# Performance work log

Measured on AMD Instinct MI355X. Metric: run time of the kernel, lower is better.

## Reference

```python
import math
import jax, jax.numpy as jnp
import numpy as np

KV_SIZE = 960
EPS = 1e-5  # InstanceNorm2d default eps


def _instance_norm(x):
    # x: [B, H, C, K]; InstanceNorm2d(affine=False): normalize each (b,h) plane
    mu = x.mean(axis=(-2, -1), keepdims=True)
    var = x.var(axis=(-2, -1), keepdims=True)  # biased variance, matches torch
    return (x - mu) * jax.lax.rsqrt(var + EPS)


def _branch(emb, Wq, K, V, Wo):
    # emb: [B,N,C], Wq: [H,C,C], K/V: [B,H,N,KV], Wo: [C,C]
    Q = jnp.einsum('bnc,hdc->bhnd', emb, Wq)                       # per-head Linear
    scores = jnp.einsum('bhnc,bhnk->bhck', Q, K) / math.sqrt(KV_SIZE)
    probs = jax.nn.softmax(_instance_norm(scores), axis=-1)        # [B,H,C,KV]
    ctx = jnp.einsum('bhck,bhnk->bhcn', probs, V)                  # [B,H,C,N]
    ctx = ctx.mean(axis=1).transpose(0, 2, 1)                      # mean over heads -> [B,N,C]
    return ctx @ Wo.T                                              # out Linear (no bias)


def setup_inputs() -> dict:
    key = jax.random.key(0)
    ks = jax.random.split(key, 16)
    B, N, H = 8, 1024, 4
    C = [64, 128, 256, 512]
    d = {}
    for i, c in enumerate(C):
        d[f'emb{i+1}'] = jax.random.normal(ks[i], (B, N, c), dtype=jnp.float32)
    d['emb_all'] = jax.random.normal(ks[4], (B, N, KV_SIZE), dtype=jnp.float32)
    for i, c in enumerate(C):
        d[f'Wq{i+1}'] = jax.random.normal(ks[5 + i], (H, c, c), dtype=jnp.float32) * 0.02
    d['Wk'] = jax.random.normal(ks[9], (H, KV_SIZE, KV_SIZE), dtype=jnp.float32) * 0.02
    d['Wv'] = jax.random.normal(ks[10], (H, KV_SIZE, KV_SIZE), dtype=jnp.float32) * 0.02
    for i, c in enumerate(C):
        d[f'Wo{i+1}'] = jax.random.normal(ks[11 + i], (c, c), dtype=jnp.float32) * 0.02
    return d


def reference(emb1, emb2, emb3, emb4, emb_all,
              Wq1, Wq2, Wq3, Wq4, Wk, Wv,
              Wo1, Wo2, Wo3, Wo4):
    # shared K/V: per-head Linear over emb_all -> [B,H,N,KV]
    K = jnp.einsum('bnk,hjk->bhnj', emb_all, Wk)
    V = jnp.einsum('bnk,hjk->bhnj', emb_all, Wv)
    O1 = _branch(emb1, Wq1, K, V, Wo1)
    O2 = _branch(emb2, Wq2, K, V, Wo2)
    O3 = _branch(emb3, Wq3, K, V, Wo3)
    O4 = _branch(emb4, Wq4, K, V, Wo4)
    return (O1, O2, O3, O4)
```

## Files before the change

### kernel.cpp

```cpp
#include <hip/hip_runtime.h>
#include <stdint.h>

typedef unsigned short u16;
typedef short bf16x8 __attribute__((ext_vector_type(8)));
typedef float f32x4 __attribute__((ext_vector_type(4)));
typedef u16 u16x4 __attribute__((ext_vector_type(4)));

__device__ __forceinline__ u16 f2bf(float f) {
    unsigned u = __builtin_bit_cast(unsigned, f);
    unsigned r = (u + 0x7fffu + ((u >> 16) & 1u)) >> 16;
    return (u16)r;
}
__device__ __forceinline__ float bf2f(u16 h) {
    unsigned u = ((unsigned)h) << 16;
    return __builtin_bit_cast(float, u);
}

typedef const __attribute__((address_space(1))) unsigned int* gptr_t;
typedef __attribute__((address_space(3))) unsigned int* lptr_t;
__device__ __forceinline__ void gload16(const void* g, void* l) {
    __builtin_amdgcn_global_load_lds((gptr_t)(uintptr_t)g, (lptr_t)(uintptr_t)l, 16, 0, 0);
}

__device__ __constant__ int d_offs[4] = {0, 512, 768, 896};
__device__ __constant__ int d_cs[4] = {512, 256, 128, 64};

__global__ __launch_bounds__(256) void cast_bf16(const float4* __restrict__ in,
                                                 u16x4* __restrict__ out, int n4) {
    int i = blockIdx.x * 256 + threadIdx.x;
    if (i < n4) {
        float4 f = in[i];
        u16x4 o = {f2bf(f.x), f2bf(f.y), f2bf(f.z), f2bf(f.w)};
        out[i] = o;
    }
}

#define ARD(DST, BUFO, Q)                                                          \
    _Pragma("unroll") for (int f = 0; f < MFP; f++)                                \
        _Pragma("unroll") for (int kb = 0; kb < 2; kb++) {                         \
            int rl = ((Q)*MFP + f) * 16 + la;                                      \
            DST[f][kb] = *(const bf16x8*)&lds[(BUFO) + rl * 64 +                   \
                                              (((kb * 4 + lk4) ^ (rl & 7)) << 3)]; \
        }
#define BRD(BUFO)                                                                  \
    _Pragma("unroll") for (int ni = 0; ni < 4; ni++)                               \
        _Pragma("unroll") for (int kb = 0; kb < 2; kb++) {                         \
            int rl = brow0 + ni * 16 + la;                                         \
            breg[ni][kb] = *(const bf16x8*)&lds[(BUFO) + rl * 64 +                 \
                                                (((kb * 4 + lk4) ^ (rl & 7)) << 3)]; \
        }
#define MMA(Q, SRC)                                                                \
    __builtin_amdgcn_sched_barrier(0);                                             \
    __builtin_amdgcn_s_setprio(1);                                                 \
    _Pragma("unroll") for (int f = 0; f < MFP; f++)                                \
        _Pragma("unroll") for (int ni = 0; ni < 4; ni++)                           \
            _Pragma("unroll") for (int kb = 0; kb < 2; kb++)                       \
                acc[(Q)*MFP + f][ni] = __builtin_amdgcn_mfma_f32_16x16x32_bf16(    \
                    SRC[f][kb], breg[ni][kb], acc[(Q)*MFP + f][ni], 0, 0, 0);      \
    __builtin_amdgcn_s_setprio(0);
#define WAITL(N) asm volatile("s_waitcnt lgkmcnt(" #N ")" ::: "memory")
#define WLGA               \
    if constexpr (MFP == 2) \
        WAITL(4);           \
    else                    \
        WAITL(2);

template <int BM>
__global__ __launch_bounds__(512, 2) void gemm_nt_8ph(
    const u16* __restrict__ A, long sAb, long sAh, int lda,
    const u16* __restrict__ B, long sBb, long sBh, int ldb,
    u16* __restrict__ C, long sCb, long sCh, int ldc,
    int M, int N, int K, int hdiv, float alpha) {
    constexpr int NA = BM / 128;
    constexpr int MFP = BM / 128;
    constexpr int WTM = BM / 2;
    constexpr int NMF = WTM / 16;
    constexpr int APART = WTM * 64;
    constexpr int BPART = 128 * 64;
    constexpr int BUFSZ = 2 * APART + 2 * BPART;
    __shared__ u16 lds[2 * BUFSZ];

    int gx = gridDim.x, gy = gridDim.y;
    int nwg = gx * gy * gridDim.z;
    int orig = blockIdx.x + gx * (blockIdx.y + gy * blockIdx.z);
    int q = nwg >> 3, r = nwg & 7;
    int xcd = orig & 7, seq = orig >> 3;
    int wg = (xcd < r ? xcd * (q + 1) : r * (q + 1) + (xcd - r) * q) + seq;
    int bx = wg % gx, tmpw = wg / gx;
    int by = tmpw % gy, bz = tmpw / gy;

    int bb = bz / hdiv, hh = bz - bb * hdiv;
    const u16* Ab = A + (size_t)bb * sAb + (size_t)hh * sAh;
    const u16* Bb = B + (size_t)bb * sBb + (size_t)hh * sBh;
    u16* Cb = C + (size_t)bb * sCb + (size_t)hh * sCh;
    int tm = by * BM, tn = bx * 256;
    int t = threadIdx.x, lane = t & 63, w = t >> 6;
    int wm = w >> 2, wn = w & 3;
    int la = lane & 15, lk4 = lane >> 4;
    int brow0 = (wn & 1) * 64;

    const u16* pA0[NA];
    const u16* pA1[NA];
    const u16* pB0[2];
    const u16* pB1[2];
#pragma unroll
    for (int i = 0; i < NA; i++) {
        int seg = i * 512 + t;
        int col = (((seg & 7) ^ ((seg >> 3) & 7)) << 3);
        int r0 = tm + (seg >> 3);
        if (r0 > M - 1) r0 = M - 1;
        pA0[i] = Ab + (size_t)r0 * lda + col;
        int r1 = tm + WTM + (seg >> 3);
        if (r1 > M - 1) r1 = M - 1;
        pA1[i] = Ab + (size_t)r1 * lda + col;
    }
#pragma unroll
    for (int i = 0; i < 2; i++) {
        int seg = i * 512 + t;
        int col = (((seg & 7) ^ ((seg >> 3) & 7)) << 3);
        int r0 = tn + (seg >> 3);
        if (r0 > N - 1) r0 = N - 1;
        pB0[i] = Bb + (size_t)r0 * ldb + col;
        int r1 = tn + 128 + (seg >> 3);
        if (r1 > N - 1) r1 = N - 1;
        pB1[i] = Bb + (size_t)r1 * ldb + col;
    }

    auto AOF = [&](int buf, int h) { return buf * BUFSZ + h * APART; };
    auto BOF = [&](int buf, int h) { return buf * BUFSZ + 2 * APART + h * BPART; };
    auto stA0 = [&](int buf) {
#pragma unroll
        for (int i = 0; i < NA; i++) {
            gload16(pA0[i], &lds[AOF(buf, 0) + (i * 512 + t) * 8]);
            pA0[i] += 64;
        }
    };
    auto stA1 = [&](int buf) {
#pragma unroll
        for (int i = 0; i < NA; i++) {
            gload16(pA1[i], &lds[AOF(buf, 1) + (i * 512 + t) * 8]);
            pA1[i] += 64;
        }
    };
    auto stB0 = [&](int buf) {
#pragma unroll
        for (int i = 0; i < 2; i++) {
            gload16(pB0[i], &lds[BOF(buf, 0) + (i * 512 + t) * 8]);
            pB0[i] += 64;
        }
    };
    auto stB1 = [&](int buf) {
#pragma unroll
        for (int i = 0; i < 2; i++) {
            gload16(pB1[i], &lds[BOF(buf, 1) + (i * 512 + t) * 8]);
            pB1[i] += 64;
        }
    };

    int nt = K / 64;
    stA0(0);
    stA1(0);
    stB0(0);
    stB1(0);
    stB0(1);
    stB1(1);
    asm volatile("s_waitcnt vmcnt(4)" ::: "memory");
    __builtin_amdgcn_s_barrier();

    f32x4 acc[NMF][4] = {};
    bf16x8 breg[4][2];
    bf16x8 aregA[MFP][2], aregB[MFP][2];
    ARD(aregA, AOF(0, wm), 0)

    for (int k = 0; k < nt; ++k) {
        int buf = k & 1, nbuf = buf ^ 1;
        int ao = AOF(buf, wm), bo = BOF(buf, wn >> 1), aoN = AOF(nbuf, wm);
        bool s1 = (k + 1 < nt), s2 = (k + 2 < nt);
        {
            __builtin_amdgcn_s_barrier();
            BRD(bo)
            ARD(aregB, ao, 1)
            if (s1) stA0(nbuf);
            WLGA
            MMA(0, aregA)
        }
        {
            __builtin_amdgcn_s_barrier();
            ARD(aregA, ao, 2)
            if (s1) stA1(nbuf);
            WLGA
            MMA(1, aregB)
        }
        {
            __builtin_amdgcn_s_barrier();
            ARD(aregB, ao, 3)
            if (s2) stB0(buf);
            WLGA
            MMA(2, aregA)
            if (s2)
                asm volatile("s_waitcnt vmcnt(2)" ::: "memory");
            else
                asm volatile("s_waitcnt vmcnt(0)" ::: "memory");
        }
        {
            __builtin_amdgcn_s_barrier();
            if (s1) { ARD(aregA, aoN, 0) }
            if (s2) stB1(buf);
            if (s1) {
                WLGA
            } else {
                WAITL(0);
            }
            MMA(3, aregB)
        }
    }
#pragma unroll
    for (int mi = 0; mi < NMF; mi++)
#pragma unroll
        for (int ni = 0; ni < 4; ni++)
#pragma unroll
            for (int r_ = 0; r_ < 4; r_++) {
                int m = tm + wm * WTM + mi * 16 + ((lane >> 4) << 2) + r_;
                int n = tn + wn * 64 + ni * 16 + la;
                if (m < M && n < N)
                    Cb[(size_t)m * ldc + n] = f2bf(acc[mi][ni][r_] * alpha);
            }
}

template <typename OUT>
__global__ __launch_bounds__(256) void gemm_nt128(
    const u16* __restrict__ A, long sAb, long sAh, int lda,
    const u16* __restrict__ B, long sBb, long sBh, int ldb,
    OUT* __restrict__ C, long sCb, long sCh, int ldc,
    int M, int N, int K, int hdiv, float alpha) {
    __shared__ u16 sA[128 * 64];
    __shared__ u16 sB[128 * 64];
    int gx = gridDim.x, gy = gridDim.y;
    int nwg = gx * gy * gridDim.z;
    int orig = blockIdx.x + gx * (blockIdx.y + gy * blockIdx.z);
    int q = nwg >> 3, r = nwg & 7;
    int xcd = orig & 7, seq = orig >> 3;
    int wg = (xcd < r ? xcd * (q + 1) : r * (q + 1) + (xcd - r) * q) + seq;
    int bx = wg % gx, tmpw = wg / gx;
    int by = tmpw % gy, bz = tmpw / gy;

    int bb = bz / hdiv, hh = bz - bb * hdiv;
    const u16* Ab = A + (size_t)bb * sAb + (size_t)hh * sAh;
    const u16* Bb = B + (size_t)bb * sBb + (size_t)hh * sBh;
    OUT* Cb = C + (size_t)bb * sCb + (size_t)hh * sCh;
    int tm = by * 128, tn = bx * 128;
    int t = threadIdx.x, lane = t & 63, w = t >> 6;
    int wr = w >> 1, wc = w & 1;
    int r0 = t >> 3, c0 = (t & 7) * 8;
    const u16* gA[4];
    const u16* gB[4];
#pragma unroll
    for (int i = 0; i < 4; i++) {
        int ar = tm + i * 32 + r0;
        if (ar > M - 1) ar = M - 1;
        gA[i] = Ab + (size_t)ar * lda + c0;
    }
#pragma unroll
    for (int i = 0; i < 4; i++) {
        int br = tn + i * 32 + r0;
        if (br > N - 1) br = N - 1;
        gB[i] = Bb + (size_t)br * ldb + c0;
    }
    f32x4 acc[4][4] = {};
    int la = lane & 15, lk = (lane >> 4) * 8;
    for (int k0 = 0; k0 < K; k0 += 64) {
#pragma unroll
        for (int i = 0; i < 4; i++) {
            gload16(gA[i], &sA[(i * 256 + t) * 8]);
            gA[i] += 64;
        }
#pragma unroll
        for (int i = 0; i < 4; i++) {
            gload16(gB[i], &sB[(i * 256 + t) * 8]);
            gB[i] += 64;
        }
        __syncthreads();
#pragma unroll
        for (int kk = 0; kk < 64; kk += 32) {
            bf16x8 a[4], b[4];
#pragma unroll
            for (int mi = 0; mi < 4; mi++)
                a[mi] = *(const bf16x8*)&sA[(wr * 64 + mi * 16 + la) * 64 + kk + lk];
#pragma unroll
            for (int ni = 0; ni < 4; ni++)
                b[ni] = *(const bf16x8*)&sB[(wc * 64 + ni * 16 + la) * 64 + kk + lk];
#pragma unroll
            for (int mi = 0; mi < 4; mi++)
#pragma unroll
                for (int ni = 0; ni < 4; ni++)
                    acc[mi][ni] = __builtin_amdgcn_mfma_f32_16x16x32_bf16(
                        a[mi], b[ni], acc[mi][ni], 0, 0, 0);
        }
        __syncthreads();
    }
#pragma unroll
    for (int mi = 0; mi < 4; mi++)
#pragma unroll
        for (int ni = 0; ni < 4; ni++)
#pragma unroll
            for (int r_ = 0; r_ < 4; r_++) {
                int m = tm + wr * 64 + mi * 16 + (lane >> 4) * 4 + r_;
                int n = tn + wc * 64 + ni * 16 + la;
                if (m < M && n < N) {
                    float v = acc[mi][ni][r_] * alpha;
                    if constexpr (sizeof(OUT) == 4)
                        Cb[(size_t)m * ldc + n] = v;
                    else
                        Cb[(size_t)m * ldc + n] = f2bf(v);
                }
            }
}

__global__ __launch_bounds__(256) void in_stats1(const u16* __restrict__ sc,
                                                 double* __restrict__ part,
                                                 int G, int mode, int C) {
    int p = blockIdx.y, g = blockIdx.x, t = threadIdx.x;
    size_t base;
    int n8;
    if (mode) {
        int z = p >> 2, i = p & 3;
        base = (size_t)z * 921600 + (size_t)d_offs[i] * 960;
        n8 = d_cs[i] * 120;
    } else {
        base = (size_t)p * C * 960;
        n8 = C * 120;
    }
    const u16* x = sc + base;
    double s = 0.0, q = 0.0;
    for (int i = g * 256 + t; i < n8; i += G * 256) {
        u16x4 a = *(const u16x4*)&x[i * 8];
        u16x4 b = *(const u16x4*)&x[i * 8 + 4];
#pragma unroll
        for (int j = 0; j < 4; j++) {
            float fa = bf2f(a[j]), fb = bf2f(b[j]);
            s += (double)fa + (double)fb;
            q += (double)fa * fa + (double)fb * fb;
        }
    }
#pragma unroll
    for (int o = 32; o; o >>= 1) {
        s += __shfl_down(s, o);
        q += __shfl_down(q, o);
    }
    __shared__ double rs[4], rq[4];
    int w = t >> 6;
    if ((t & 63) == 0) {
        rs[w] = s;
        rq[w] = q;
    }
    __syncthreads();
    if (t == 0) {
        part[2 * ((size_t)p * G + g)] = rs[0] + rs[1] + rs[2] + rs[3];
        part[2 * ((size_t)p * G + g) + 1] = rq[0] + rq[1] + rq[2] + rq[3];
    }
}

__global__ __launch_bounds__(64) void in_stats2(const double* __restrict__ part,
                                                float* __restrict__ stats,
                                                int G, int mode, int C) {
    int p = blockIdx.x, t = threadIdx.x;
    int cnt = (mode ? d_cs[p & 3] : C) * 960;
    double s = 0.0, q = 0.0;
    if (t < G) {
        s = part[2 * ((size_t)p * G + t)];
        q = part[2 * ((size_t)p * G + t) + 1];
    }
#pragma unroll
    for (int o = 32; o; o >>= 1) {
        s += __shfl_down(s, o);
        q += __shfl_down(q, o);
    }
    if (t == 0) {
        float mu = (float)(s / cnt);
        float var = (float)(q / cnt) - mu * mu;
        stats[2 * p] = mu;
        stats[2 * p + 1] = rsqrtf(var + 1e-5f);
    }
}

__global__ __launch_bounds__(256) void norm_softmax_cat(const u16* __restrict__ sc,
                                                        const float* __restrict__ stats,
                                                        u16* __restrict__ prB) {
    int row = blockIdx.x;
    int z = row / 960, c = row - z * 960;
    int i = c < 512 ? 0 : (c < 768 ? 1 : (c < 896 ? 2 : 3));
    int plane = z * 4 + i;
    int b = z >> 2, h = z & 3;
    const u16* x = sc + (size_t)row * 960;
    u16* o = prB + (((size_t)b * 960 + c) * 4 + h) * 960;
    float mu = stats[2 * plane], rs = stats[2 * plane + 1];
    int t = threadIdx.x;
    bool act = t < 240;
    float v[4];
    float mx = -1e30f;
    if (act) {
        u16x4 d = *(const u16x4*)&x[t * 4];
#pragma unroll
        for (int j = 0; j < 4; j++) {
            v[j] = (bf2f(d[j]) - mu) * rs;
            mx = fmaxf(mx, v[j]);
        }
    }
    __shared__ float r1[4], r2[4];
#pragma unroll
    for (int o_ = 32; o_; o_ >>= 1) mx = fmaxf(mx, __shfl_xor(mx, o_));
    int w = t >> 6;
    if ((t & 63) == 0) r1[w] = mx;
    __syncthreads();
    mx = fmaxf(fmaxf(r1[0], r1[1]), fmaxf(r1[2], r1[3]));
    float s = 0.f;
    if (act) {
#pragma unroll
        for (int j = 0; j < 4; j++) {
            v[j] = __expf(v[j] - mx);
            s += v[j];
        }
    }
#pragma unroll
    for (int o_ = 32; o_; o_ >>= 1) s += __shfl_xor(s, o_);
    if ((t & 63) == 0) r2[w] = s;
    __syncthreads();
    s = r2[0] + r2[1] + r2[2] + r2[3];
    float inv = 1.0f / s;
    if (act) {
        u16x4 ov;
#pragma unroll
        for (int j = 0; j < 4; j++) ov[j] = f2bf(v[j] * inv);
        *(u16x4*)&o[t * 4] = ov;
    }
}

__global__ __launch_bounds__(256) void norm_softmax_ip(u16* sc,
                                                       const float* __restrict__ stats,
                                                       int C) {
    int row = blockIdx.x;
    int plane = row / C;
    u16* x = sc + (size_t)row * 960;
    float mu = stats[2 * plane], rs = stats[2 * plane + 1];
    int t = threadIdx.x;
    bool act = t < 240;
    float v[4];
    float mx = -1e30f;
    if (act) {
        u16x4 d = *(const u16x4*)&x[t * 4];
#pragma unroll
        for (int j = 0; j < 4; j++) {
            v[j] = (bf2f(d[j]) - mu) * rs;
            mx = fmaxf(mx, v[j]);
        }
    }
    __shared__ float r1[4], r2[4];
#pragma unroll
    for (int o = 32; o; o >>= 1) mx = fmaxf(mx, __shfl_xor(mx, o));
    int w = t >> 6;
    if ((t & 63) == 0) r1[w] = mx;
    __syncthreads();
    mx = fmaxf(fmaxf(r1[0], r1[1]), fmaxf(r1[2], r1[3]));
    float s = 0.f;
    if (act) {
#pragma unroll
        for (int j = 0; j < 4; j++) {
            v[j] = __expf(v[j] - mx);
            s += v[j];
        }
    }
#pragma unroll
    for (int o = 32; o; o >>= 1) s += __shfl_xor(s, o);
    if ((t & 63) == 0) r2[w] = s;
    __syncthreads();
    s = r2[0] + r2[1] + r2[2] + r2[3];
    float inv = 1.0f / s;
    if (act) {
        u16x4 o;
#pragma unroll
        for (int j = 0; j < 4; j++) o[j] = f2bf(v[j] * inv);
        *(u16x4*)&x[t * 4] = o;
    }
}

__global__ __launch_bounds__(256) void mean_heads(const u16* __restrict__ ctx, long ps,
                                                  u16* __restrict__ cm, int C) {
    int b = blockIdx.z;
    int n0 = blockIdx.x * 64, c0 = blockIdx.y * 64;
    __shared__ float sm[64][65];
    int t = threadIdx.x;
    float acc[16];
#pragma unroll
    for (int j = 0; j < 16; j++) acc[j] = 0.f;
    for (int h = 0; h < 4; h++) {
        const u16* p = ctx + (size_t)(b * 4 + h) * ps;
#pragma unroll
        for (int j = 0; j < 16; j++) {
            int lin = j * 256 + t;
            int cc = lin >> 6, nn = lin & 63;
            acc[j] += bf2f(p[(size_t)(c0 + cc) * 1024 + n0 + nn]);
        }
    }
#pragma unroll
    for (int j = 0; j < 16; j++) {
        int lin = j * 256 + t;
        sm[lin >> 6][lin & 63] = acc[j] * 0.25f;
    }
    __syncthreads();
#pragma unroll
    for (int j = 0; j < 16; j++) {
        int lin = j * 256 + t;
        int nn = lin >> 6, cc = lin & 63;
        cm[((size_t)b * 1024 + n0 + nn) * C + c0 + cc] = f2bf(sm[cc][nn]);
    }
}

extern "C" void kernel_launch(void* const* d_in, const int* in_sizes, int n_in,
                              void* d_out, int out_size, void* d_ws, size_t ws_size,
                              hipStream_t stream) {
    const int B = 8, NN = 1024, KV = 960;
    const int Cs[4] = {64, 128, 256, 512};
    const int ord[4] = {3, 2, 1, 0};
    const int offs[4] = {0, 512, 768, 896};
    const float* emb[4];
    for (int i = 0; i < 4; i++) emb[i] = (const float*)d_in[i];
    const float* embAll = (const float*)d_in[4];
    const float* Wq[4];
    for (int i = 0; i < 4; i++) Wq[i] = (const float*)d_in[5 + i];
    const float* Wk = (const float*)d_in[9];
    const float* Wv = (const float*)d_in[10];
    const float* Wo[4];
    for (int i = 0; i < 4; i++) Wo[i] = (const float*)d_in[11 + i];
    float* out = (float*)d_out;
    size_t outOff[4];
    {
        size_t o = 0;
        for (int i = 0; i < 4; i++) { outOff[i] = o; o += (size_t)B * NN * Cs[i]; }
    }

    const size_t SKV = 62914560;
    const size_t SSC = 58982400;
    const size_t SWQ = 2785280, SWO = 696320, SCM = 8388608;
    const size_t SPART = 131072, SST = 1024;
    const size_t SMALL = SWQ + SWO + SCM + SPART + SST;
    const size_t NEED_BAT = SSC + 3 * SKV + SMALL + 512;

    float invs = 1.0f / sqrtf((float)KV);
    auto g128 = [](int n) { return (n + 127) / 128; };

    if (ws_size >= NEED_BAT) {
        char* p = (char*)d_ws;
        u16* scB = (u16*)p;        p += SSC;
        u16* QtB = (u16*)p;        p += SKV;
        u16* Kt = (u16*)p;         p += SKV;
        u16* VbC = (u16*)p;        p += SKV;
        u16* wq[4];
        for (int i = 0; i < 4; i++) { wq[i] = (u16*)p; p += (size_t)4 * Cs[i] * Cs[i] * 2; }
        u16* wo[4];
        for (int i = 0; i < 4; i++) { wo[i] = (u16*)p; p += (size_t)Cs[i] * Cs[i] * 2; }
        u16* cmX = (u16*)p;        p += SCM;
        double* part = (double*)p; p += SPART;
        float* stats = (float*)p;

        u16* eA = scB;
        u16* wk = (u16*)((char*)scB + 15728640);
        u16* wv = (u16*)((char*)scB + 23101440);
        u16* prB = QtB;
        u16* cmC = scB;

        auto castL = [&](const float* s, u16* d, size_t n) {
            int n4 = (int)(n / 4);
            cast_bf16<<<(n4 + 255) / 256, 256, 0, stream>>>((const float4*)s, (u16x4*)d, n4);
        };
        castL(embAll, eA, (size_t)B * NN * KV);
        castL(Wk, wk, (size_t)4 * KV * KV);
        castL(Wv, wv, (size_t)4 * KV * KV);
        for (int i = 0; i < 4; i++) castL(Wq[i], wq[i], (size_t)4 * Cs[i] * Cs[i]);
        for (int i = 0; i < 4; i++) castL(Wo[i], wo[i], (size_t)Cs[i] * Cs[i]);

        gemm_nt_8ph<256><<<dim3(4, 4, 32), 512, 0, stream>>>(
            wk, 0, (long)KV * KV, KV, eA, (long)NN * KV, 0, KV,
            Kt, 4 * 983040L, 983040L, NN, KV, NN, KV, 4, 1.0f);
        gemm_nt_8ph<256><<<dim3(4, 4, 32), 512, 0, stream>>>(
            eA, (long)NN * KV, 0, KV, wv, 0, (long)KV * KV, KV,
            VbC, (long)NN * 3840, 960L, 3840, NN, KV, KV, 4, 1.0f);

        for (int j = 0; j < 4; j++) {
            int i = ord[j], C = Cs[i];
            castL(emb[i], cmX, (size_t)B * NN * C);
            if (C == 512) {
                gemm_nt_8ph<256><<<dim3(4, 2, 32), 512, 0, stream>>>(
                    wq[i], 0, (long)C * C, C, cmX, (long)NN * C, 0, C,
                    QtB + (size_t)offs[j] * 1024, 4 * 983040L, 983040L, NN,
                    C, NN, C, 4, 1.0f);
            } else {
                gemm_nt128<u16><<<dim3(8, g128(C), 32), 256, 0, stream>>>(
                    wq[i], 0, (long)C * C, C, cmX, (long)NN * C, 0, C,
                    QtB + (size_t)offs[j] * 1024, 4 * 983040L, 983040L, NN,
                    C, NN, C, 4, 1.0f);
            }
        }
        gemm_nt_8ph<256><<<dim3(4, 4, 32), 512, 0, stream>>>(
            QtB, 983040L, 0, NN, Kt, 983040L, 0, NN,
            scB, 921600L, 0, KV, 960, KV, NN, 1, invs);
        in_stats1<<<dim3(16, 128), 256, 0, stream>>>(scB, part, 16, 1, 0);
        in_stats2<<<128, 64, 0, stream>>>(part, stats, 16, 1, 0);
        norm_softmax_cat<<<32 * 960, 256, 0, stream>>>(scB, stats, prB);
        gemm_nt_8ph<128><<<dim3(4, 8, 8), 512, 0, stream>>>(
            VbC, (long)NN * 3840, 0, 3840, prB, (long)960 * 3840, 0, 3840,
            cmC, (long)NN * 960, 0, 960, NN, 960, 3840, 1, 0.25f);
        for (int j = 0; j < 4; j++) {
            int i = ord[j], C = Cs[i];
            gemm_nt128<float><<<dim3(g128(C), 8, 8), 256, 0, stream>>>(
                cmC + offs[j], (long)NN * 960, 0, 960, wo[i], 0, 0, C,
                out + outOff[i], (long)NN * C, 0, C, NN, C, C, 1, 1.0f);
        }
    } else {
        const size_t S1 = 33554432, S2 = 33554432;
        if (ws_size < S1 + S2 + 2 * SKV + SMALL + 512) return;
        char* p = (char*)d_ws;
        char* buf1 = p;            p += S1;
        char* buf2 = p;            p += S2;
        u16* Kt = (u16*)p;         p += SKV;
        u16* Vb = (u16*)p;         p += SKV;
        u16* wq[4];
        for (int i = 0; i < 4; i++) { wq[i] = (u16*)p; p += (size_t)4 * Cs[i] * Cs[i] * 2; }
        u16* wo[4];
        for (int i = 0; i < 4; i++) { wo[i] = (u16*)p; p += (size_t)Cs[i] * Cs[i] * 2; }
        u16* cmX = (u16*)p;        p += SCM;
        double* part = (double*)p; p += SPART;
        float* stats = (float*)p;

        u16* eA = (u16*)buf1;
        u16* wk = (u16*)(buf1 + 15728640);
        u16* wv = (u16*)(buf1 + 23101440);
        u16* sc = (u16*)buf1;
        u16* Qt = (u16*)buf2;
        u16* ctx = (u16*)buf2;

        auto castL = [&](const float* s, u16* d, size_t n) {
            int n4 = (int)(n / 4);
            cast_bf16<<<(n4 + 255) / 256, 256, 0, stream>>>((const float4*)s, (u16x4*)d, n4);
        };
        castL(embAll, eA, (size_t)B * NN * KV);
        castL(Wk, wk, (size_t)4 * KV * KV);
        castL(Wv, wv, (size_t)4 * KV * KV);
        for (int i = 0; i < 4; i++) castL(Wq[i], wq[i], (size_t)4 * Cs[i] * Cs[i]);
        for (int i = 0; i < 4; i++) castL(Wo[i], wo[i], (size_t)Cs[i] * Cs[i]);

        gemm_nt128<u16><<<dim3(8, 8, 32), 256, 0, stream>>>(
            wk, 0, (long)KV * KV, KV, eA, (long)NN * KV, 0, KV,
            Kt, 4 * 983040L, 983040L, NN, KV, NN, KV, 4, 1.0f);
        gemm_nt128<u16><<<dim3(8, 8, 32), 256, 0, stream>>>(
            eA, (long)NN * KV, 0, KV, wv, 0, (long)KV * KV, KV,
            Vb, 4 * 983040L, 983040L, KV, NN, KV, KV, 4, 1.0f);

        for (int i = 0; i < 4; i++) {
            int C = Cs[i];
            castL(emb[i], cmX, (size_t)B * NN * C);
            gemm_nt128<u16><<<dim3(8, g128(C), 32), 256, 0, stream>>>(
                wq[i], 0, (long)C * C, C, cmX, (long)NN * C, 0, C,
                Qt, 4L * C * NN, (long)C * NN, NN, C, NN, C, 4, 1.0f);
            gemm_nt128<u16><<<dim3(8, g128(C), 32), 256, 0, stream>>>(
                Qt, (long)C * NN, 0, NN, Kt, 983040L, 0, NN,
                sc, (long)C * KV, 0, KV, C, KV, NN, 1, invs);
            in_stats1<<<dim3(64, 32), 256, 0, stream>>>(sc, part, 64, 0, C);
            in_stats2<<<32, 64, 0, stream>>>(part, stats, 64, 0, C);
            norm_softmax_ip<<<32 * C, 256, 0, stream>>>(sc, stats, C);
            gemm_nt128<u16><<<dim3(8, g128(C), 32), 256, 0, stream>>>(
                sc, (long)C * KV, 0, KV, Vb, 983040L, 0, KV,
                ctx, (long)C * NN, 0, NN, C, NN, KV, 1, 1.0f);
            mean_heads<<<dim3(16, C / 64, B), 256, 0, stream>>>(
                ctx, (long)C * NN, cmX, C);
            gemm_nt128<float><<<dim3(g128(C), 8, B), 256, 0, stream>>>(
                cmX, (long)NN * C, 0, C, wo[i], 0, 0, C,
                out + outOff[i], (long)NN * C, 0, C, NN, C, C, 1, 1.0f);
        }
    }
}
```

Measured before the change: 472.6 us.

## Replace 8-phase GEMM main loop with simpler 2-half schedule

```diff
diff --git a/kernel.cpp b/kernel.cpp
--- a/kernel.cpp
+++ b/kernel.cpp
@@ -35,10 +35,10 @@
     }
 }
 
-#define ARD(DST, BUFO, Q)                                                          \
-    _Pragma("unroll") for (int f = 0; f < MFP; f++)                                \
+#define ARDH(DST, BUFO, H)                                                         \
+    _Pragma("unroll") for (int f = 0; f < HMF; f++)                                \
         _Pragma("unroll") for (int kb = 0; kb < 2; kb++) {                         \
-            int rl = ((Q)*MFP + f) * 16 + la;                                      \
+            int rl = ((H)*HMF + f) * 16 + la;                                      \
             DST[f][kb] = *(const bf16x8*)&lds[(BUFO) + rl * 64 +                   \
                                               (((kb * 4 + lk4) ^ (rl & 7)) << 3)]; \
         }
@@ -49,32 +49,27 @@
             breg[ni][kb] = *(const bf16x8*)&lds[(BUFO) + rl * 64 +                 \
                                                 (((kb * 4 + lk4) ^ (rl & 7)) << 3)]; \
         }
-#define MMA(Q, SRC)                                                                \
+#define MMAH(H, SRC)                                                               \
     __builtin_amdgcn_sched_barrier(0);                                             \
     __builtin_amdgcn_s_setprio(1);                                                 \
-    _Pragma("unroll") for (int f = 0; f < MFP; f++)                                \
+    _Pragma("unroll") for (int f = 0; f < HMF; f++)                                \
         _Pragma("unroll") for (int ni = 0; ni < 4; ni++)                           \
             _Pragma("unroll") for (int kb = 0; kb < 2; kb++)                       \
-                acc[(Q)*MFP + f][ni] = __builtin_amdgcn_mfma_f32_16x16x32_bf16(    \
-                    SRC[f][kb], breg[ni][kb], acc[(Q)*MFP + f][ni], 0, 0, 0);      \
+                acc[(H)*HMF + f][ni] = __builtin_amdgcn_mfma_f32_16x16x32_bf16(    \
+                    SRC[f][kb], breg[ni][kb], acc[(H)*HMF + f][ni], 0, 0, 0);      \
     __builtin_amdgcn_s_setprio(0);
-#define WAITL(N) asm volatile("s_waitcnt lgkmcnt(" #N ")" ::: "memory")
-#define WLGA               \
-    if constexpr (MFP == 2) \
-        WAITL(4);           \
-    else                    \
-        WAITL(2);
+#define WLG0 asm volatile("s_waitcnt lgkmcnt(0)" ::: "memory")
 
 template <int BM>
-__global__ __launch_bounds__(512, 2) void gemm_nt_8ph(
+__global__ __launch_bounds__(512, 2) void gemm_nt_4ph(
     const u16* __restrict__ A, long sAb, long sAh, int lda,
     const u16* __restrict__ B, long sBb, long sBh, int ldb,
     u16* __restrict__ C, long sCb, long sCh, int ldc,
     int M, int N, int K, int hdiv, float alpha) {
     constexpr int NA = BM / 128;
-    constexpr int MFP = BM / 128;
     constexpr int WTM = BM / 2;
     constexpr int NMF = WTM / 16;
+    constexpr int HMF = NMF / 2;
     constexpr int APART = WTM * 64;
     constexpr int BPART = 128 * 64;
     constexpr int BUFSZ = 2 * APART + 2 * BPART;
@@ -162,57 +157,44 @@
     stA1(0);
     stB0(0);
     stB1(0);
-    stB0(1);
-    stB1(1);
-    asm volatile("s_waitcnt vmcnt(4)" ::: "memory");
+    if (nt > 1) {
+        stB0(1);
+        stB1(1);
+        asm volatile("s_waitcnt vmcnt(4)" ::: "memory");
+    } else {
+        asm volatile("s_waitcnt vmcnt(0)" ::: "memory");
+    }
     __builtin_amdgcn_s_barrier();
 
     f32x4 acc[NMF][4] = {};
     bf16x8 breg[4][2];
-    bf16x8 aregA[MFP][2], aregB[MFP][2];
-    ARD(aregA, AOF(0, wm), 0)
+    bf16x8 aLo[HMF][2], aHi[HMF][2];
 
     for (int k = 0; k < nt; ++k) {
         int buf = k & 1, nbuf = buf ^ 1;
-        int ao = AOF(buf, wm), bo = BOF(buf, wn >> 1), aoN = AOF(nbuf, wm);
+        int ao = AOF(buf, wm), bo = BOF(buf, wn >> 1);
         bool s1 = (k + 1 < nt), s2 = (k + 2 < nt);
-        {
-            __builtin_amdgcn_s_barrier();
-            BRD(bo)
-            ARD(aregB, ao, 1)
-            if (s1) stA0(nbuf);
-            WLGA
-            MMA(0, aregA)
-        }
-        {
-            __builtin_amdgcn_s_barrier();
-            ARD(aregA, ao, 2)
-            if (s1) stA1(nbuf);
-            WLGA
-            MMA(1, aregB)
-        }
-        {
-            __builtin_amdgcn_s_barrier();
-            ARD(aregB, ao, 3)
-            if (s2) stB0(buf);
-            WLGA
-            MMA(2, aregA)
-            if (s2)
-                asm volatile("s_waitcnt vmcnt(2)" ::: "memory");
-            else
-                asm volatile("s_waitcnt vmcnt(0)" ::: "memory");
-        }
-        {
-            __builtin_amdgcn_s_barrier();
-            if (s1) { ARD(aregA, aoN, 0) }
-            if (s2) stB1(buf);
-            if (s1) {
-                WLGA
-            } else {
-                WAITL(0);
-            }
-            MMA(3, aregB)
-        }
+        BRD(bo)
+        ARDH(aLo, ao, 0)
+        if (s1) {
+            stA0(nbuf);
+            stA1(nbuf);
+        }
+        WLG0;
+        MMAH(0, aLo)
+        ARDH(aHi, ao, 1)
+        __builtin_amdgcn_s_barrier();
+        if (s2) {
+            stB0(buf);
+            stB1(buf);
+        }
+        WLG0;
+        MMAH(1, aHi)
+        if (s2)
+            asm volatile("s_waitcnt vmcnt(4)" ::: "memory");
+        else
+            asm volatile("s_waitcnt vmcnt(0)" ::: "memory");
+        __builtin_amdgcn_s_barrier();
     }
 #pragma unroll
     for (int mi = 0; mi < NMF; mi++)
@@ -578,10 +560,10 @@
         for (int i = 0; i < 4; i++) castL(Wq[i], wq[i], (size_t)4 * Cs[i] * Cs[i]);
         for (int i = 0; i < 4; i++) castL(Wo[i], wo[i], (size_t)Cs[i] * Cs[i]);
 
-        gemm_nt_8ph<256><<<dim3(4, 4, 32), 512, 0, stream>>>(
+        gemm_nt_4ph<256><<<dim3(4, 4, 32), 512, 0, stream>>>(
             wk, 0, (long)KV * KV, KV, eA, (long)NN * KV, 0, KV,
             Kt, 4 * 983040L, 983040L, NN, KV, NN, KV, 4, 1.0f);
-        gemm_nt_8ph<256><<<dim3(4, 4, 32), 512, 0, stream>>>(
+        gemm_nt_4ph<256><<<dim3(4, 4, 32), 512, 0, stream>>>(
             eA, (long)NN * KV, 0, KV, wv, 0, (long)KV * KV, KV,
             VbC, (long)NN * 3840, 960L, 3840, NN, KV, KV, 4, 1.0f);
 
@@ -589,7 +571,7 @@
             int i = ord[j], C = Cs[i];
             castL(emb[i], cmX, (size_t)B * NN * C);
             if (C == 512) {
-                gemm_nt_8ph<256><<<dim3(4, 2, 32), 512, 0, stream>>>(
+                gemm_nt_4ph<256><<<dim3(4, 2, 32), 512, 0, stream>>>(
                     wq[i], 0, (long)C * C, C, cmX, (long)NN * C, 0, C,
                     QtB + (size_t)offs[j] * 1024, 4 * 983040L, 983040L, NN,
                     C, NN, C, 4, 1.0f);
@@ -600,13 +582,13 @@
                     C, NN, C, 4, 1.0f);
             }
         }
-        gemm_nt_8ph<256><<<dim3(4, 4, 32), 512, 0, stream>>>(
+        gemm_nt_4ph<256><<<dim3(4, 4, 32), 512, 0, stream>>>(
             QtB, 983040L, 0, NN, Kt, 983040L, 0, NN,
             scB, 921600L, 0, KV, 960, KV, NN, 1, invs);
         in_stats1<<<dim3(16, 128), 256, 0, stream>>>(scB, part, 16, 1, 0);
         in_stats2<<<128, 64, 0, stream>>>(part, stats, 16, 1, 0);
         norm_softmax_cat<<<32 * 960, 256, 0, stream>>>(scB, stats, prB);
-        gemm_nt_8ph<128><<<dim3(4, 8, 8), 512, 0, stream>>>(
+        gemm_nt_4ph<128><<<dim3(4, 8, 8), 512, 0, stream>>>(
             VbC, (long)NN * 3840, 0, 3840, prB, (long)960 * 3840, 0, 3840,
             cmC, (long)NN * 960, 0, 960, NN, 960, 3840, 1, 0.25f);
         for (int j = 0; j < 4; j++) {
```

New measurement: 454.3 us. -3.9%, faster.
